# Kernel optimization log

Measured on AMD Instinct MI355X. Metric: run time of the kernel, lower is better.

Reference implementation:

```python
import jax, jax.numpy as jnp
import numpy as np

HEADS = 16
LN_EPS = 1e-12
MINUS_INF = -10000.0  # matches DeepSpeed's minus_inf constant


def setup_inputs() -> dict:
    key = jax.random.key(0)
    ks = jax.random.split(key, 6)
    B, S, H = 2, 2048, 2048
    x = jax.random.normal(ks[0], (B, S, H), dtype=jnp.float32)
    mask = jnp.zeros((B, 1, 1, S), dtype=jnp.float32)  # additive float mask (no padding)
    qkvw = jax.random.normal(ks[1], (H, 3 * H), dtype=jnp.float32) * 0.02
    qkvb = jax.random.normal(ks[2], (3 * H,), dtype=jnp.float32) * 0.02
    ow = jax.random.normal(ks[3], (H, H), dtype=jnp.float32) * 0.02
    norm_w = jnp.ones((H,), dtype=jnp.float32)
    norm_b = jnp.zeros((H,), dtype=jnp.float32)
    return {"x": x, "mask": mask, "qkvw": qkvw, "qkvb": qkvb, "ow": ow,
            "norm_w": norm_w, "norm_b": norm_b}


def _layernorm(x, g, b):
    mu = jnp.mean(x, axis=-1, keepdims=True)
    var = jnp.mean(jnp.square(x - mu), axis=-1, keepdims=True)
    return (x - mu) * jax.lax.rsqrt(var + LN_EPS) * g + b


def reference(x, mask, qkvw, qkvb, ow, norm_w, norm_b):
    B, S, H = x.shape
    dh = H // HEADS
    # QKVGemmOp: fused layernorm + QKV projection
    inp_norm = _layernorm(x, norm_w, norm_b)                      # [B,S,H]
    qkv = jnp.einsum('bsh,he->bse', inp_norm, qkvw) + qkvb        # [B,S,3H]
    q, k, v = jnp.split(qkv, 3, axis=-1)
    q = q.reshape(B, S, HEADS, dh).transpose(0, 2, 1, 3)          # [B,Hd,S,dh]
    k = k.reshape(B, S, HEADS, dh).transpose(0, 2, 1, 3)
    v = v.reshape(B, S, HEADS, dh).transpose(0, 2, 1, 3)
    # SoftmaxContextOp: kernel scales q and k each by 1/norm_factor,
    # norm_factor = d_head**0.25 (use_mup=False) -> net scale 1/sqrt(d_head)
    scale = 1.0 / jnp.sqrt(jnp.asarray(dh, dtype=x.dtype))
    scores = jnp.einsum('bhqd,bhkd->bhqk', q, k) * scale          # [B,Hd,S,S]
    causal = jnp.tril(jnp.ones((S, S), dtype=bool))
    scores = jnp.where(causal[None, None], scores + mask, MINUS_INF)
    probs = jax.nn.softmax(scores, axis=-1)
    ctx = jnp.einsum('bhqk,bhkd->bhqd', probs, v)                 # [B,Hd,S,dh]
    ctx = ctx.transpose(0, 2, 1, 3).reshape(B, S, H)
    # VectorMatMulOp: output projection (no bias here)
    out = jnp.einsum('bsh,ho->bso', ctx, ow)                      # [B,S,H]
    return (out, k, v, ctx, inp_norm)
```

## Files before the change

### kernel.cpp

```cpp
#include <hip/hip_runtime.h>

typedef short bf16x8 __attribute__((ext_vector_type(8)));
typedef float floatx4 __attribute__((ext_vector_type(4)));

#define MFMA16(a, b, c) __builtin_amdgcn_mfma_f32_16x16x32_bf16((a), (b), (c), 0, 0, 0)

__device__ __forceinline__ unsigned short f2bf(float f) {
    union { float f; unsigned int u; } v; v.f = f;
    unsigned int u = v.u;
    return (unsigned short)((u + 0x7FFFu + ((u >> 16) & 1u)) >> 16);
}

__device__ __forceinline__ void gld_lds16(const void* g, void* l) {
    __builtin_amdgcn_global_load_lds(
        (const __attribute__((address_space(1))) unsigned int*)g,
        (__attribute__((address_space(3))) unsigned int*)l, 16, 0, 0);
}

__global__ __launch_bounds__(256) void ln_kernel(
        const float* __restrict__ x, const float* __restrict__ g,
        const float* __restrict__ be, float* __restrict__ yo,
        unsigned short* __restrict__ yb) {
    int row = blockIdx.x, t = threadIdx.x;
    const float* xr = x + (size_t)row * 2048;
    float4 a = ((const float4*)xr)[2 * t];
    float4 b = ((const float4*)xr)[2 * t + 1];
    float s = a.x + a.y + a.z + a.w + b.x + b.y + b.z + b.w;
    float q = a.x * a.x + a.y * a.y + a.z * a.z + a.w * a.w +
              b.x * b.x + b.y * b.y + b.z * b.z + b.w * b.w;
    for (int m = 1; m < 64; m <<= 1) { s += __shfl_xor(s, m); q += __shfl_xor(q, m); }
    __shared__ float red[8];
    if ((t & 63) == 0) { red[t >> 6] = s; red[4 + (t >> 6)] = q; }
    __syncthreads();
    s = red[0] + red[1] + red[2] + red[3];
    q = red[4] + red[5] + red[6] + red[7];
    float mean = s * (1.0f / 2048.0f);
    float var = q * (1.0f / 2048.0f) - mean * mean;
    float rs = rsqrtf(var + 1e-12f);
    float4 g0 = ((const float4*)g)[2 * t], g1 = ((const float4*)g)[2 * t + 1];
    float4 b0 = ((const float4*)be)[2 * t], b1 = ((const float4*)be)[2 * t + 1];
    float4 y0, y1;
    y0.x = (a.x - mean) * rs * g0.x + b0.x;
    y0.y = (a.y - mean) * rs * g0.y + b0.y;
    y0.z = (a.z - mean) * rs * g0.z + b0.z;
    y0.w = (a.w - mean) * rs * g0.w + b0.w;
    y1.x = (b.x - mean) * rs * g1.x + b1.x;
    y1.y = (b.y - mean) * rs * g1.y + b1.y;
    y1.z = (b.z - mean) * rs * g1.z + b1.z;
    y1.w = (b.w - mean) * rs * g1.w + b1.w;
    float* yr = yo + (size_t)row * 2048;
    ((float4*)yr)[2 * t] = y0;
    ((float4*)yr)[2 * t + 1] = y1;
    union { unsigned short u[8]; uint4 v; } pk;
    pk.u[0] = f2bf(y0.x); pk.u[1] = f2bf(y0.y); pk.u[2] = f2bf(y0.z); pk.u[3] = f2bf(y0.w);
    pk.u[4] = f2bf(y1.x); pk.u[5] = f2bf(y1.y); pk.u[6] = f2bf(y1.z); pk.u[7] = f2bf(y1.w);
    *(uint4*)(yb + (size_t)row * 2048 + t * 8) = pk.v;
}

__global__ __launch_bounds__(256) void transpose_cvt(
        const float* __restrict__ src, unsigned short* __restrict__ dst,
        int K, int N) {
    __shared__ unsigned short tile[64][73];
    int n0 = blockIdx.x * 64, k0 = blockIdx.y * 64;
    size_t bo = (size_t)blockIdx.z * K * N;
    int t = threadIdx.x;
    for (int p = 0; p < 4; p++) {
        int idx = p * 256 + t; int r = idx >> 4; int c = (idx & 15) * 4;
        float4 v = *(const float4*)(src + bo + (size_t)(k0 + r) * N + n0 + c);
        tile[r][c] = f2bf(v.x); tile[r][c + 1] = f2bf(v.y);
        tile[r][c + 2] = f2bf(v.z); tile[r][c + 3] = f2bf(v.w);
    }
    __syncthreads();
    for (int p = 0; p < 4; p++) {
        int idx = p * 256 + t; int n = idx >> 4; int c = (idx & 15) * 4;
        ushort4 o;
        o.x = tile[c][n]; o.y = tile[c + 1][n];
        o.z = tile[c + 2][n]; o.w = tile[c + 3][n];
        *(ushort4*)(dst + bo + (size_t)(n0 + n) * K + k0 + c) = o;
    }
}

__global__ __launch_bounds__(256) void gemm_qkv(
        const unsigned short* __restrict__ A, const unsigned short* __restrict__ Bt,
        const float* __restrict__ bias, float* __restrict__ ko,
        float* __restrict__ vo, unsigned short* __restrict__ qws,
        unsigned short* __restrict__ kbf) {
    __shared__ unsigned short As[128 * 64];
    __shared__ unsigned short Bs[128 * 64];
    int m0 = blockIdx.y * 128, n0 = blockIdx.x * 128;
    int t = threadIdx.x;
    int wave = t >> 6, lane = t & 63, ln15 = lane & 15, quad = lane >> 4;
    int wm = wave >> 1, wn = wave & 1;
    floatx4 acc[4][4] = {};
    for (int k0 = 0; k0 < 2048; k0 += 64) {
        for (int p = 0; p < 4; p++) {
            int idx = p * 256 + t; int r = idx >> 3; int c = (idx & 7) * 8;
            gld_lds16(A + (size_t)(m0 + r) * 2048 + k0 + c, As + p * 2048 + wave * 512);
            gld_lds16(Bt + (size_t)(n0 + r) * 2048 + k0 + c, Bs + p * 2048 + wave * 512);
        }
        __syncthreads();
        for (int ks = 0; ks < 2; ks++) {
            bf16x8 af[4], bfr[4];
            for (int i = 0; i < 4; i++)
                af[i] = *(const bf16x8*)&As[(wm * 64 + i * 16 + ln15) * 64 + ks * 32 + quad * 8];
            for (int i = 0; i < 4; i++)
                bfr[i] = *(const bf16x8*)&Bs[(wn * 64 + i * 16 + ln15) * 64 + ks * 32 + quad * 8];
            for (int mi = 0; mi < 4; mi++)
                for (int ni = 0; ni < 4; ni++)
                    acc[mi][ni] = MFMA16(af[mi], bfr[ni], acc[mi][ni]);
        }
        __syncthreads();
    }
    for (int mi = 0; mi < 4; mi++) {
        int row = m0 + wm * 64 + mi * 16 + quad * 4;
        for (int ni = 0; ni < 4; ni++) {
            int col = n0 + wn * 64 + ni * 16 + ln15;
            float bv = bias[col];
            for (int r = 0; r < 4; r++) {
                float val = acc[mi][ni][r] + bv;
                int rr = row + r;
                int b = rr >> 11, s = rr & 2047;
                if (col < 2048) {
                    qws[(size_t)rr * 2048 + col] = f2bf(val);
                } else if (col < 4096) {
                    int cc = col - 2048; int h = cc >> 7, d = cc & 127;
                    size_t o = ((size_t)(b * 16 + h) * 2048 + s) * 128 + d;
                    ko[o] = val;
                    kbf[o] = f2bf(val);
                } else {
                    int cc = col - 4096; int h = cc >> 7, d = cc & 127;
                    vo[((size_t)(b * 16 + h) * 2048 + s) * 128 + d] = val;
                }
            }
        }
    }
}

__global__ __launch_bounds__(256) void gemm_out(
        const float* __restrict__ Actx, const unsigned short* __restrict__ Bt,
        float* __restrict__ out) {
    __shared__ unsigned short As[128 * 72];
    __shared__ unsigned short Bs[128 * 72];
    int m0 = blockIdx.y * 128, n0 = blockIdx.x * 128;
    int t = threadIdx.x;
    int wave = t >> 6, lane = t & 63, ln15 = lane & 15, quad = lane >> 4;
    int wm = wave >> 1, wn = wave & 1;
    floatx4 acc[4][4] = {};
    for (int k0 = 0; k0 < 2048; k0 += 64) {
        for (int p = 0; p < 4; p++) {
            int idx = p * 256 + t; int r = idx >> 3; int c = (idx & 7) * 8;
            const float* ap = Actx + (size_t)(m0 + r) * 2048 + k0 + c;
            float4 u0 = ((const float4*)ap)[0], u1 = ((const float4*)ap)[1];
            union { unsigned short u[8]; uint4 v; } pk;
            pk.u[0] = f2bf(u0.x); pk.u[1] = f2bf(u0.y); pk.u[2] = f2bf(u0.z); pk.u[3] = f2bf(u0.w);
            pk.u[4] = f2bf(u1.x); pk.u[5] = f2bf(u1.y); pk.u[6] = f2bf(u1.z); pk.u[7] = f2bf(u1.w);
            *(uint4*)&As[r * 72 + c] = pk.v;
            *(uint4*)&Bs[r * 72 + c] = *(const uint4*)(Bt + (size_t)(n0 + r) * 2048 + k0 + c);
        }
        __syncthreads();
        for (int ks = 0; ks < 2; ks++) {
            bf16x8 af[4], bfr[4];
            for (int i = 0; i < 4; i++)
                af[i] = *(const bf16x8*)&As[(wm * 64 + i * 16 + ln15) * 72 + ks * 32 + quad * 8];
            for (int i = 0; i < 4; i++)
                bfr[i] = *(const bf16x8*)&Bs[(wn * 64 + i * 16 + ln15) * 72 + ks * 32 + quad * 8];
            for (int mi = 0; mi < 4; mi++)
                for (int ni = 0; ni < 4; ni++)
                    acc[mi][ni] = MFMA16(af[mi], bfr[ni], acc[mi][ni]);
        }
        __syncthreads();
    }
    for (int mi = 0; mi < 4; mi++) {
        int row = m0 + wm * 64 + mi * 16 + quad * 4;
        for (int ni = 0; ni < 4; ni++) {
            int col = n0 + wn * 64 + ni * 16 + ln15;
            for (int r = 0; r < 4; r++)
                out[(size_t)(row + r) * 2048 + col] = acc[mi][ni][r];
        }
    }
}

__global__ __launch_bounds__(256) void attn_kernel(
        const unsigned short* __restrict__ qws, const unsigned short* __restrict__ kbf,
        const unsigned short* __restrict__ vT, const float* __restrict__ mask,
        float* __restrict__ ctxo) {
    __shared__ unsigned short Ks[64 * 136];
    __shared__ unsigned short Vt[128 * 72];
    __shared__ unsigned short Pl[4 * 16 * 72];
    int jp = blockIdx.x, h = blockIdx.y, b = blockIdx.z;
    int t = threadIdx.x, wave = t >> 6, lane = t & 63, ln15 = lane & 15, quad = lane >> 4;
    const float scale = 0.08838834764831845f;

    const unsigned short* kb = kbf + (size_t)(b * 16 + h) * 2048 * 128;
    const unsigned short* vTb = vT + (size_t)(b * 16 + h) * 128 * 2048;
    const float* mb = mask + (size_t)b * 2048;

    for (int half = 0; half < 2; half++) {
        int qt = half ? (31 - jp) : jp;
        int Q0 = qt * 64;

        bf16x8 qf[4];
        const unsigned short* qbase =
            qws + ((size_t)(b * 2048 + Q0 + wave * 16 + ln15)) * 2048 + h * 128;
        for (int ks = 0; ks < 4; ks++)
            qf[ks] = *(const bf16x8*)(qbase + ks * 32 + quad * 8);

        float m_r[4], l_r[4];
        floatx4 o[8] = {};
        for (int r = 0; r < 4; r++) { m_r[r] = -1e30f; l_r[r] = 0.0f; }

        int nkt = qt + 1;
        for (int kt = 0; kt < nkt; kt++) {
            int c0 = kt * 64;
            for (int p = 0; p < 4; p++) {
                int idx = p * 256 + t; int r = idx >> 4; int c = (idx & 15) * 8;
                *(uint4*)&Ks[r * 136 + c] = *(const uint4*)(kb + (size_t)(c0 + r) * 128 + c);
            }
            for (int p = 0; p < 4; p++) {
                int idx = p * 256 + t; int d = idx >> 3; int sg = (idx & 7) * 8;
                *(uint4*)&Vt[d * 72 + sg] = *(const uint4*)(vTb + (size_t)d * 2048 + c0 + sg);
            }
            __syncthreads();

            floatx4 cs[4] = {};
            for (int ks = 0; ks < 4; ks++)
                for (int ni = 0; ni < 4; ni++) {
                    bf16x8 kfr = *(const bf16x8*)&Ks[(ni * 16 + ln15) * 136 + ks * 32 + quad * 8];
                    cs[ni] = MFMA16(qf[ks], kfr, cs[ni]);
                }

            float sv[4][4];
            float mt[4] = {-1e30f, -1e30f, -1e30f, -1e30f};
            if (kt == qt) {
                for (int ni = 0; ni < 4; ni++) {
                    int cg = c0 + ni * 16 + ln15;
                    float mk = mb[cg];
                    for (int r = 0; r < 4; r++) {
                        int qg = Q0 + wave * 16 + quad * 4 + r;
                        float v = (cg <= qg) ? cs[ni][r] * scale + mk : -10000.0f;
                        sv[ni][r] = v;
                        mt[r] = fmaxf(mt[r], v);
                    }
                }
            } else {
                for (int ni = 0; ni < 4; ni++) {
                    float mk = mb[c0 + ni * 16 + ln15];
                    for (int r = 0; r < 4; r++) {
                        float v = cs[ni][r] * scale + mk;
                        sv[ni][r] = v;
                        mt[r] = fmaxf(mt[r], v);
                    }
                }
            }
            for (int m = 1; m < 16; m <<= 1)
                for (int r = 0; r < 4; r++) mt[r] = fmaxf(mt[r], __shfl_xor(mt[r], m));
            float alpha[4], lt[4];
            for (int r = 0; r < 4; r++) {
                float mn = fmaxf(m_r[r], mt[r]);
                alpha[r] = __expf(m_r[r] - mn);
                m_r[r] = mn;
                lt[r] = 0.0f;
            }
            for (int ni = 0; ni < 4; ni++)
                for (int r = 0; r < 4; r++) {
                    float p = __expf(sv[ni][r] - m_r[r]);
                    sv[ni][r] = p;
                    lt[r] += p;
                }
            for (int m = 1; m < 16; m <<= 1)
                for (int r = 0; r < 4; r++) lt[r] += __shfl_xor(lt[r], m);
            for (int r = 0; r < 4; r++) l_r[r] = l_r[r] * alpha[r] + lt[r];
            for (int nj = 0; nj < 8; nj++)
                for (int r = 0; r < 4; r++) o[nj][r] *= alpha[r];

            unsigned short* pw = &Pl[wave * 16 * 72];
            for (int ni = 0; ni < 4; ni++)
                for (int r = 0; r < 4; r++)
                    pw[(quad * 4 + r) * 72 + ni * 16 + ln15] = f2bf(sv[ni][r]);

            for (int ks2 = 0; ks2 < 2; ks2++) {
                bf16x8 pf = *(const bf16x8*)&Pl[(wave * 16 + ln15) * 72 + ks2 * 32 + quad * 8];
                for (int nj = 0; nj < 8; nj++) {
                    bf16x8 vf = *(const bf16x8*)&Vt[(nj * 16 + ln15) * 72 + ks2 * 32 + quad * 8];
                    o[nj] = MFMA16(pf, vf, o[nj]);
                }
            }
            __syncthreads();
        }

        float rl[4];
        for (int r = 0; r < 4; r++) rl[r] = 1.0f / l_r[r];
        for (int nj = 0; nj < 8; nj++)
            for (int r = 0; r < 4; r++) {
                int s = Q0 + wave * 16 + quad * 4 + r;
                ctxo[((size_t)(b * 2048 + s)) * 2048 + h * 128 + nj * 16 + ln15] = o[nj][r] * rl[r];
            }
    }
}

extern "C" void kernel_launch(void* const* d_in, const int* in_sizes, int n_in,
                              void* d_out, int out_size, void* d_ws, size_t ws_size,
                              hipStream_t stream) {
    const float* x      = (const float*)d_in[0];
    const float* mask   = (const float*)d_in[1];
    const float* qkvw   = (const float*)d_in[2];
    const float* qkvb   = (const float*)d_in[3];
    const float* ow     = (const float*)d_in[4];
    const float* norm_w = (const float*)d_in[5];
    const float* norm_b = (const float*)d_in[6];

    float* out      = (float*)d_out;
    float* k_out    = out + 8388608;
    float* v_out    = out + 16777216;
    float* ctx_out  = out + 25165824;
    float* norm_out = out + 33554432;

    unsigned short* ws    = (unsigned short*)d_ws;
    unsigned short* xn    = ws;
    unsigned short* qkvwT = ws + 8388608;
    unsigned short* owT   = ws + 8388608 + 12582912;
    unsigned short* qws   = owT + 4194304;
    unsigned short* vT    = qws + 8388608;
    unsigned short* kbf   = vT + 8388608;

    ln_kernel<<<4096, 256, 0, stream>>>(x, norm_w, norm_b, norm_out, xn);
    transpose_cvt<<<dim3(96, 32, 1), 256, 0, stream>>>(qkvw, qkvwT, 2048, 6144);
    transpose_cvt<<<dim3(32, 32, 1), 256, 0, stream>>>(ow, owT, 2048, 2048);
    gemm_qkv<<<dim3(48, 32), 256, 0, stream>>>(xn, qkvwT, qkvb, k_out, v_out, qws, kbf);
    transpose_cvt<<<dim3(2, 32, 32), 256, 0, stream>>>(v_out, vT, 2048, 128);
    attn_kernel<<<dim3(16, 16, 2), 256, 0, stream>>>(qws, kbf, vT, mask, ctx_out);
    gemm_out<<<dim3(16, 32), 256, 0, stream>>>(ctx_out, owT, out);
}
```

Before: 560.8 us.

## Rewrite QKV GEMM with 256x256 tiles, double-buffered LDS pipeline and swizzle

The QKV projection GEMM moves from 128x128 tiles with 4 waves and a synchronous load/compute loop to 256x256 tiles with 8 waves and double-buffered LDS. Global-to-LDS loads for later k-tiles are interleaved with MFMA phases, using explicit barriers, waitcnt and setprio. LDS accesses use an XOR swizzle to avoid bank conflicts, and the block index is remapped so neighbouring blocks share tiles in L2. The intent is to hide memory latency and raise MFMA utilisation, at the cost of more LDS and registers per block and fragile hand-written synchronisation.

```diff
diff --git a/kernel.cpp b/kernel.cpp
--- a/kernel.cpp
+++ b/kernel.cpp
@@ -80,42 +80,174 @@
     }
 }
 
-__global__ __launch_bounds__(256) void gemm_qkv(
+#define NT_QKV 32
+
+__device__ __forceinline__ void stage_A(const unsigned short* __restrict__ Ag,
+        unsigned short* As, int mh, int m0, int kt, int tid) {
+#pragma unroll
+    for (int j = 0; j < 2; j++) {
+        int G = j * 512 + tid;
+        int s = (G >> 3) & 63;
+        int gr = G & 7;
+        int row = j * 128 + mh * 64 + s;
+        const unsigned short* src =
+            Ag + (size_t)(m0 + row) * 2048 + kt * 64 + ((gr ^ (s & 7)) << 3);
+        unsigned short* dst = As + j * 8192 + mh * 4096 + (tid >> 6) * 512;
+        gld_lds16(src, dst);
+    }
+}
+
+__device__ __forceinline__ void stage_B(const unsigned short* __restrict__ Bg,
+        unsigned short* Bs, int nh, int n0, int kt, int tid) {
+#pragma unroll
+    for (int j = 0; j < 2; j++) {
+        int G = j * 512 + tid;
+        int wcc = G >> 8;
+        int s = (G >> 3) & 31;
+        int gr = G & 7;
+        int row = wcc * 64 + nh * 32 + s;
+        const unsigned short* src =
+            Bg + (size_t)(n0 + row) * 2048 + kt * 64 + ((gr ^ (s & 7)) << 3);
+        unsigned short* dst = Bs + wcc * 4096 + nh * 2048 + ((tid >> 6) & 3) * 512;
+        gld_lds16(src, dst);
+    }
+}
+
+__device__ __forceinline__ bf16x8 ldfrag(const unsigned short* S, int row, int ks,
+                                         int quad, int ln15) {
+    int gr = ((ks << 2) | quad) ^ (ln15 & 7);
+    return *(const bf16x8*)(S + row * 64 + gr * 8);
+}
+
+__device__ __forceinline__ void qkv_tile(
+        const unsigned short* __restrict__ Ag, const unsigned short* __restrict__ Bg,
+        unsigned short* Asc, unsigned short* Bsc,
+        unsigned short* Asn, unsigned short* Bsn,
+        int t, int m0, int n0, int tid, int wr, int wc, int ln15, int quad,
+        floatx4 (&acc)[8][4]) {
+    bf16x8 a[4][2], bb[2][2];
+#pragma unroll
+    for (int m = 0; m < 4; m++) {
+        a[m][0] = ldfrag(Asc, wr * 128 + m * 16 + ln15, 0, quad, ln15);
+        a[m][1] = ldfrag(Asc, wr * 128 + m * 16 + ln15, 1, quad, ln15);
+    }
+#pragma unroll
+    for (int n = 0; n < 2; n++) {
+        bb[n][0] = ldfrag(Bsc, wc * 64 + n * 16 + ln15, 0, quad, ln15);
+        bb[n][1] = ldfrag(Bsc, wc * 64 + n * 16 + ln15, 1, quad, ln15);
+    }
+    if (t + 1 < NT_QKV) stage_B(Bg, Bsn, 0, n0, t + 1, tid);
+    __builtin_amdgcn_s_barrier();
+    asm volatile("s_waitcnt lgkmcnt(0)" ::: "memory");
+    __builtin_amdgcn_sched_barrier(0);
+    __builtin_amdgcn_s_setprio(1);
+#pragma unroll
+    for (int m = 0; m < 4; m++)
+#pragma unroll
+        for (int n = 0; n < 2; n++) {
+            acc[m][n] = MFMA16(a[m][0], bb[n][0], acc[m][n]);
+            acc[m][n] = MFMA16(a[m][1], bb[n][1], acc[m][n]);
+        }
+    __builtin_amdgcn_s_setprio(0);
+    __builtin_amdgcn_s_barrier();
+#pragma unroll
+    for (int n = 0; n < 2; n++) {
+        bb[n][0] = ldfrag(Bsc, wc * 64 + (2 + n) * 16 + ln15, 0, quad, ln15);
+        bb[n][1] = ldfrag(Bsc, wc * 64 + (2 + n) * 16 + ln15, 1, quad, ln15);
+    }
+    if (t + 2 < NT_QKV) stage_A(Ag, Asc, 0, m0, t + 2, tid);
+    __builtin_amdgcn_s_barrier();
+    asm volatile("s_waitcnt lgkmcnt(0)" ::: "memory");
+    __builtin_amdgcn_sched_barrier(0);
+    __builtin_amdgcn_s_setprio(1);
+#pragma unroll
+    for (int m = 0; m < 4; m++)
+#pragma unroll
+        for (int n = 0; n < 2; n++) {
+            acc[m][2 + n] = MFMA16(a[m][0], bb[n][0], acc[m][2 + n]);
+            acc[m][2 + n] = MFMA16(a[m][1], bb[n][1], acc[m][2 + n]);
+        }
+    __builtin_amdgcn_s_setprio(0);
+    __builtin_amdgcn_s_barrier();
+#pragma unroll
+    for (int m = 0; m < 4; m++) {
+        a[m][0] = ldfrag(Asc, wr * 128 + (4 + m) * 16 + ln15, 0, quad, ln15);
+        a[m][1] = ldfrag(Asc, wr * 128 + (4 + m) * 16 + ln15, 1, quad, ln15);
+    }
+    if (t + 2 < NT_QKV) stage_B(Bg, Bsc, 1, n0, t + 2, tid);
+    __builtin_amdgcn_s_barrier();
+    asm volatile("s_waitcnt lgkmcnt(0)" ::: "memory");
+    __builtin_amdgcn_sched_barrier(0);
+    __builtin_amdgcn_s_setprio(1);
+#pragma unroll
+    for (int m = 0; m < 4; m++)
+#pragma unroll
+        for (int n = 0; n < 2; n++) {
+            acc[4 + m][2 + n] = MFMA16(a[m][0], bb[n][0], acc[4 + m][2 + n]);
+            acc[4 + m][2 + n] = MFMA16(a[m][1], bb[n][1], acc[4 + m][2 + n]);
+        }
+    __builtin_amdgcn_s_setprio(0);
+    __builtin_amdgcn_s_barrier();
+#pragma unroll
+    for (int n = 0; n < 2; n++) {
+        bb[n][0] = ldfrag(Bsc, wc * 64 + n * 16 + ln15, 0, quad, ln15);
+        bb[n][1] = ldfrag(Bsc, wc * 64 + n * 16 + ln15, 1, quad, ln15);
+    }
+    if (t + 2 < NT_QKV) stage_A(Ag, Asc, 1, m0, t + 2, tid);
+    __builtin_amdgcn_s_barrier();
+    asm volatile("s_waitcnt lgkmcnt(0)" ::: "memory");
+    __builtin_amdgcn_sched_barrier(0);
+    __builtin_amdgcn_s_setprio(1);
+#pragma unroll
+    for (int m = 0; m < 4; m++)
+#pragma unroll
+        for (int n = 0; n < 2; n++) {
+            acc[4 + m][n] = MFMA16(a[m][0], bb[n][0], acc[4 + m][n]);
+            acc[4 + m][n] = MFMA16(a[m][1], bb[n][1], acc[4 + m][n]);
+        }
+    __builtin_amdgcn_s_setprio(0);
+    if (t + 2 < NT_QKV) asm volatile("s_waitcnt vmcnt(6)" ::: "memory");
+    else                asm volatile("s_waitcnt vmcnt(0)" ::: "memory");
+    __builtin_amdgcn_s_barrier();
+}
+
+__global__ __launch_bounds__(512, 2) void gemm_qkv(
         const unsigned short* __restrict__ A, const unsigned short* __restrict__ Bt,
         const float* __restrict__ bias, float* __restrict__ ko,
         float* __restrict__ vo, unsigned short* __restrict__ qws,
         unsigned short* __restrict__ kbf) {
-    __shared__ unsigned short As[128 * 64];
-    __shared__ unsigned short Bs[128 * 64];
-    int m0 = blockIdx.y * 128, n0 = blockIdx.x * 128;
-    int t = threadIdx.x;
-    int wave = t >> 6, lane = t & 63, ln15 = lane & 15, quad = lane >> 4;
-    int wm = wave >> 1, wn = wave & 1;
-    floatx4 acc[4][4] = {};
-    for (int k0 = 0; k0 < 2048; k0 += 64) {
-        for (int p = 0; p < 4; p++) {
-            int idx = p * 256 + t; int r = idx >> 3; int c = (idx & 7) * 8;
-            gld_lds16(A + (size_t)(m0 + r) * 2048 + k0 + c, As + p * 2048 + wave * 512);
-            gld_lds16(Bt + (size_t)(n0 + r) * 2048 + k0 + c, Bs + p * 2048 + wave * 512);
-        }
-        __syncthreads();
-        for (int ks = 0; ks < 2; ks++) {
-            bf16x8 af[4], bfr[4];
-            for (int i = 0; i < 4; i++)
-                af[i] = *(const bf16x8*)&As[(wm * 64 + i * 16 + ln15) * 64 + ks * 32 + quad * 8];
-            for (int i = 0; i < 4; i++)
-                bfr[i] = *(const bf16x8*)&Bs[(wn * 64 + i * 16 + ln15) * 64 + ks * 32 + quad * 8];
-            for (int mi = 0; mi < 4; mi++)
-                for (int ni = 0; ni < 4; ni++)
-                    acc[mi][ni] = MFMA16(af[mi], bfr[ni], acc[mi][ni]);
-        }
-        __syncthreads();
-    }
-    for (int mi = 0; mi < 4; mi++) {
-        int row = m0 + wm * 64 + mi * 16 + quad * 4;
+    __shared__ __align__(16) unsigned short As[2][16384];
+    __shared__ __align__(16) unsigned short Bs[2][16384];
+    int bid = blockIdx.x;
+    int wg = (bid & 7) * 48 + (bid >> 3);
+    int mt = wg / 24, ntile = wg % 24;
+    int m0 = mt * 256, n0 = ntile * 256;
+    int tid = threadIdx.x;
+    int wave = tid >> 6, lane = tid & 63, ln15 = lane & 15, quad = lane >> 4;
+    int wr = wave >> 2, wc = wave & 3;
+    floatx4 acc[8][4] = {};
+    stage_B(Bt, Bs[0], 0, n0, 0, tid);
+    stage_A(A, As[0], 0, m0, 0, tid);
+    stage_B(Bt, Bs[0], 1, n0, 0, tid);
+    stage_A(A, As[0], 1, m0, 0, tid);
+    stage_A(A, As[1], 0, m0, 1, tid);
+    stage_B(Bt, Bs[1], 1, n0, 1, tid);
+    stage_A(A, As[1], 1, m0, 1, tid);
+    asm volatile("s_waitcnt vmcnt(6)" ::: "memory");
+    __builtin_amdgcn_s_barrier();
+#pragma unroll 1
+    for (int t = 0; t < NT_QKV; t += 2) {
+        qkv_tile(A, Bt, As[0], Bs[0], As[1], Bs[1], t,     m0, n0, tid, wr, wc, ln15, quad, acc);
+        qkv_tile(A, Bt, As[1], Bs[1], As[0], Bs[0], t + 1, m0, n0, tid, wr, wc, ln15, quad, acc);
+    }
+#pragma unroll
+    for (int mi = 0; mi < 8; mi++) {
+        int row = m0 + wr * 128 + mi * 16 + quad * 4;
+#pragma unroll
         for (int ni = 0; ni < 4; ni++) {
-            int col = n0 + wn * 64 + ni * 16 + ln15;
+            int col = n0 + wc * 64 + ni * 16 + ln15;
             float bv = bias[col];
+#pragma unroll
             for (int r = 0; r < 4; r++) {
                 float val = acc[mi][ni][r] + bv;
                 int rr = row + r;
@@ -326,7 +458,7 @@
     ln_kernel<<<4096, 256, 0, stream>>>(x, norm_w, norm_b, norm_out, xn);
     transpose_cvt<<<dim3(96, 32, 1), 256, 0, stream>>>(qkvw, qkvwT, 2048, 6144);
     transpose_cvt<<<dim3(32, 32, 1), 256, 0, stream>>>(ow, owT, 2048, 2048);
-    gemm_qkv<<<dim3(48, 32), 256, 0, stream>>>(xn, qkvwT, qkvb, k_out, v_out, qws, kbf);
+    gemm_qkv<<<dim3(384), 512, 0, stream>>>(xn, qkvwT, qkvb, k_out, v_out, qws, kbf);
     transpose_cvt<<<dim3(2, 32, 32), 256, 0, stream>>>(v_out, vT, 2048, 128);
     attn_kernel<<<dim3(16, 16, 2), 256, 0, stream>>>(qws, kbf, vT, mask, ctx_out);
     gemm_out<<<dim3(16, 32), 256, 0, stream>>>(ctx_out, owT, out);
```

After: 543.9 us. 3.0% less time.
